# Kernel optimization log

Measured on AMD Instinct MI355X. Metric: run time of the kernel, lower is better.

The kernel has to match this reference:

```python
import jax, jax.numpy as jnp
import numpy as np

N, F, F_, H = 8192, 1024, 64, 4
LEAKY_ALPHA = 0.2
MASK_VAL = -1e10


def setup_inputs() -> dict:
    key = jax.random.key(0)
    k1, k2, k3, k4 = jax.random.split(key, 4)
    X = jax.random.normal(k1, (N, F), dtype=jnp.float32)
    # sparse-ish binary adjacency with self loops (A = A + I in the source script)
    A = (jax.random.uniform(k2, (N, N)) < 0.004).astype(jnp.float32)
    A = jnp.clip(A + jnp.eye(N, dtype=jnp.float32), 0.0, 1.0)
    W = jax.random.normal(k3, (H, F, F_), dtype=jnp.float32) * (1.0 / np.sqrt(F))
    attn_a = jax.random.normal(k4, (H, 2 * F_, 1), dtype=jnp.float32) * (1.0 / np.sqrt(2 * F_))
    bias = jnp.zeros((H, F_), dtype=jnp.float32)
    return {"X": X, "A": A, "W": W, "attn_a": attn_a, "bias": bias}


def reference(X, A, W, attn_a, bias):
    # features per head: [H, N, F_]
    feats = jnp.einsum('nf,hfk->hnk', X, W)
    # concat-score trick: [f_i, f_j] @ a == f_i @ a[:F_] + f_j @ a[F_:]
    a_self = attn_a[:, :F_, 0]   # [H, F_]
    a_neigh = attn_a[:, F_:, 0]  # [H, F_]
    s_self = jnp.einsum('hnk,hk->hn', feats, a_self)   # [H, N]
    s_neigh = jnp.einsum('hnk,hk->hn', feats, a_neigh)  # [H, N]
    scores = s_self[:, :, None] + s_neigh[:, None, :]   # [H, N, N]
    scores = jnp.where(scores > 0, scores, LEAKY_ALPHA * scores)  # LeakyReLU(0.2)
    scores = scores + MASK_VAL * (1.0 - A)[None]
    attn = jax.nn.softmax(scores, axis=-1)              # [H, N, N]
    # aggregate (dropout is identity at inference)
    out = jnp.einsum('hij,hjk->hik', attn, feats) + bias[:, None, :]  # [H, N, F_]
    out = jnp.transpose(out, (1, 0, 2)).reshape(X.shape[0], H * F_)   # concat heads
    return jax.nn.relu(out)
```

## Files before the change

kernel.cpp:

```cpp
#include <hip/hip_runtime.h>
#include <hip/hip_bf16.h>
#include <stdint.h>

#define NN 8192
#define FF 1024
#define FD 64
#define NH 4
#define CC 256
#define MAXE 192

typedef __attribute__((ext_vector_type(8))) short short8;
typedef __attribute__((ext_vector_type(4))) short short4v;
typedef __attribute__((ext_vector_type(4))) float f32x4;

__device__ __forceinline__ short bf16_rne(float f) {
    union { float f; uint32_t u; } v; v.f = f;
    uint32_t r = (v.u + 0x7FFFu + ((v.u >> 16) & 1u)) >> 16;
    return (short)(r & 0xFFFFu);
}
__device__ __forceinline__ float bf2f(short s) {
    union { uint32_t u; float f; } v; v.u = ((uint32_t)(uint16_t)s) << 16;
    return v.f;
}

__global__ __launch_bounds__(256) void scan_kernel(const float* __restrict__ A,
                                                   int* __restrict__ nbr,
                                                   int* __restrict__ cnt) {
    __shared__ int idx[MAXE];
    __shared__ int c;
    const int row = blockIdx.x;
    const int t = threadIdx.x;
    if (t == 0) c = 0;
    __syncthreads();
    const f32x4* A4 = (const f32x4*)(A + (size_t)row * NN);
    for (int r = 0; r < 8; ++r) {
        int c4 = r * 256 + t;
        f32x4 v = __builtin_nontemporal_load(&A4[c4]);
        if (v.x > 0.5f) { int p = atomicAdd(&c, 1); if (p < MAXE) idx[p] = c4 * 4 + 0; }
        if (v.y > 0.5f) { int p = atomicAdd(&c, 1); if (p < MAXE) idx[p] = c4 * 4 + 1; }
        if (v.z > 0.5f) { int p = atomicAdd(&c, 1); if (p < MAXE) idx[p] = c4 * 4 + 2; }
        if (v.w > 0.5f) { int p = atomicAdd(&c, 1); if (p < MAXE) idx[p] = c4 * 4 + 3; }
    }
    __syncthreads();
    int n = min(c, MAXE);
    if (t < n) nbr[row * MAXE + t] = idx[t];
    if (t == 0) cnt[row] = n;
}

__global__ __launch_bounds__(256) void wt_kernel(const float* __restrict__ W,
                                                 short* __restrict__ Wt) {
    int gid = blockIdx.x * 256 + threadIdx.x;
    int k = gid & 1023;
    int n = (gid >> 10) & 63;
    int h = gid >> 16;
    Wt[gid] = bf16_rne(W[(h << 16) + k * 64 + n]);
}

__global__ __launch_bounds__(256) void xb_kernel(const float* __restrict__ X,
                                                 short* __restrict__ Xb) {
    int gid = blockIdx.x * 256 + threadIdx.x;
    float4 v = ((const float4*)X)[gid];
    short4 o;
    o.x = bf16_rne(v.x); o.y = bf16_rne(v.y);
    o.z = bf16_rne(v.z); o.w = bf16_rne(v.w);
    ((short4*)Xb)[gid] = o;
}

__global__ __launch_bounds__(256) void gemm_kernel(const short* __restrict__ Xb,
                                                   const short* __restrict__ Wt,
                                                   const float* __restrict__ attn_a,
                                                   short* __restrict__ featb,
                                                   float* __restrict__ s_self,
                                                   float* __restrict__ s_neigh) {
    __shared__ short Xs[64 * 40];
    __shared__ short Ws[64 * 40];
    const int h  = blockIdx.x;
    const int m0 = blockIdx.y * 64;
    const int t  = threadIdx.x;
    const int wave = t >> 6, lane = t & 63;
    const int q = lane >> 4, nl = lane & 15;
    const int srow = t >> 2, sk8 = (t & 3) * 8;

    f32x4 acc0 = {0.f,0.f,0.f,0.f}, acc1 = {0.f,0.f,0.f,0.f};
    f32x4 acc2 = {0.f,0.f,0.f,0.f}, acc3 = {0.f,0.f,0.f,0.f};

    const short* Xp = Xb + (size_t)(m0 + srow) * FF + sk8;
    const short* Wp = Wt + (size_t)(h * 64 + srow) * FF + sk8;

    for (int k0 = 0; k0 < FF; k0 += 32) {
        short8 xv = *(const short8*)(Xp + k0);
        short8 wv = *(const short8*)(Wp + k0);
        *(short8*)(&Xs[srow * 40 + sk8]) = xv;
        *(short8*)(&Ws[srow * 40 + sk8]) = wv;
        __syncthreads();
        short8 a  = *(const short8*)(&Xs[(wave * 16 + nl) * 40 + q * 8]);
        short8 b0 = *(const short8*)(&Ws[( 0 + nl) * 40 + q * 8]);
        short8 b1 = *(const short8*)(&Ws[(16 + nl) * 40 + q * 8]);
        short8 b2 = *(const short8*)(&Ws[(32 + nl) * 40 + q * 8]);
        short8 b3 = *(const short8*)(&Ws[(48 + nl) * 40 + q * 8]);
        acc0 = __builtin_amdgcn_mfma_f32_16x16x32_bf16(a, b0, acc0, 0, 0, 0);
        acc1 = __builtin_amdgcn_mfma_f32_16x16x32_bf16(a, b1, acc1, 0, 0, 0);
        acc2 = __builtin_amdgcn_mfma_f32_16x16x32_bf16(a, b2, acc2, 0, 0, 0);
        acc3 = __builtin_amdgcn_mfma_f32_16x16x32_bf16(a, b3, acc3, 0, 0, 0);
        __syncthreads();
    }
    const int row = m0 + wave * 16 + q * 4;
    const int colbase = h * 64 + nl;
    for (int r = 0; r < 4; ++r) {
        short* fr = featb + (size_t)(row + r) * CC + colbase;
        fr[ 0] = bf16_rne(acc0[r]);
        fr[16] = bf16_rne(acc1[r]);
        fr[32] = bf16_rne(acc2[r]);
        fr[48] = bf16_rne(acc3[r]);
    }
    const float A0 = attn_a[h * 128 + nl],      A1 = attn_a[h * 128 + nl + 16];
    const float A2 = attn_a[h * 128 + nl + 32], A3 = attn_a[h * 128 + nl + 48];
    const float B0 = attn_a[h * 128 + 64 + nl],      B1 = attn_a[h * 128 + 64 + nl + 16];
    const float B2 = attn_a[h * 128 + 64 + nl + 32], B3 = attn_a[h * 128 + 64 + nl + 48];
    for (int r = 0; r < 4; ++r) {
        float ps = acc0[r] * A0 + acc1[r] * A1 + acc2[r] * A2 + acc3[r] * A3;
        float pn = acc0[r] * B0 + acc1[r] * B1 + acc2[r] * B2 + acc3[r] * B3;
        for (int off = 1; off < 16; off <<= 1) {
            ps += __shfl_xor(ps, off);
            pn += __shfl_xor(pn, off);
        }
        if (nl == 0) {
            s_self [h * NN + row + r] = ps;
            s_neigh[h * NN + row + r] = pn;
        }
    }
}

__global__ __launch_bounds__(256) void smax_kernel(const int* __restrict__ nbr,
                                                   const int* __restrict__ cnt,
                                                   const short* __restrict__ featb,
                                                   const float* __restrict__ s_self,
                                                   const float* __restrict__ s_neigh,
                                                   const float* __restrict__ bias,
                                                   float* __restrict__ out) {
    __shared__ int js[MAXE];
    __shared__ float ps[NH][MAXE];
    const int row = blockIdx.x;
    const int t = threadIdx.x;
    const int h = t >> 6, lane = t & 63;
    const int n = cnt[row];
    if (t < n) js[t] = nbr[row * MAXE + t];
    __syncthreads();

    const float si = s_self[h * NN + row];
    const float* snh = s_neigh + h * NN;

    float sc[3];
    #pragma unroll
    for (int i = 0; i < 3; ++i) {
        int e = lane + 64 * i;
        float s = -1e30f;
        if (e < n) {
            s = si + snh[js[e]];
            s = s > 0.f ? s : 0.2f * s;
        }
        sc[i] = s;
    }
    float m = fmaxf(sc[0], fmaxf(sc[1], sc[2]));
    for (int off = 1; off < 64; off <<= 1) m = fmaxf(m, __shfl_xor(m, off));

    float dsum = 0.f;
    #pragma unroll
    for (int i = 0; i < 3; ++i) {
        int e = lane + 64 * i;
        if (e < n) {
            float p = __expf(sc[i] - m);
            ps[h][e] = p;
            dsum += p;
        }
    }
    for (int off = 1; off < 64; off <<= 1) dsum += __shfl_xor(dsum, off);

    const int sub = lane >> 4;
    const int l16 = lane & 15;
    const short* fb = featb + h * 64 + l16 * 4;
    f32x4 acc = {0.f, 0.f, 0.f, 0.f};
    #pragma unroll 2
    for (int e = sub; e < n; e += 4) {
        int j = js[e];
        float p = ps[h][e];
        short4v f = *(const short4v*)(fb + (size_t)j * CC);
        acc[0] = fmaf(p, bf2f(f.x), acc[0]);
        acc[1] = fmaf(p, bf2f(f.y), acc[1]);
        acc[2] = fmaf(p, bf2f(f.z), acc[2]);
        acc[3] = fmaf(p, bf2f(f.w), acc[3]);
    }
    #pragma unroll
    for (int k = 0; k < 4; ++k) {
        acc[k] += __shfl_xor(acc[k], 16);
        acc[k] += __shfl_xor(acc[k], 32);
    }
    if (sub == 0) {
        float rd = 1.0f / dsum;
        f32x4 o;
        #pragma unroll
        for (int k = 0; k < 4; ++k)
            o[k] = fmaxf(acc[k] * rd + bias[h * 64 + l16 * 4 + k], 0.f);
        *(f32x4*)(out + (size_t)row * CC + h * 64 + l16 * 4) = o;
    }
}

extern "C" void kernel_launch(void* const* d_in, const int* in_sizes, int n_in,
                              void* d_out, int out_size, void* d_ws, size_t ws_size,
                              hipStream_t stream) {
    const float* X      = (const float*)d_in[0];
    const float* A      = (const float*)d_in[1];
    const float* W      = (const float*)d_in[2];
    const float* attn_a = (const float*)d_in[3];
    const float* bias   = (const float*)d_in[4];
    float* out = (float*)d_out;

    char* ws = (char*)d_ws;
    short* featb   = (short*)ws;
    float* s_self  = (float*)(ws + 4194304);
    float* s_neigh = (float*)(ws + 4325376);
    short* Wt      = (short*)(ws + 4456448);
    short* Xb      = (short*)(ws + 4980736);
    int*   nbr     = (int*)  (ws + 21757952);
    int*   cnt     = (int*)  (ws + 28049408);

    scan_kernel<<<NN, 256, 0, stream>>>(A, nbr, cnt);
    wt_kernel  <<<1024, 256, 0, stream>>>(W, Wt);
    xb_kernel  <<<8192, 256, 0, stream>>>(X, Xb);
    gemm_kernel<<<dim3(4, 128), 256, 0, stream>>>(Xb, Wt, attn_a, featb, s_self, s_neigh);
    smax_kernel<<<NN, 256, 0, stream>>>(nbr, cnt, featb, s_self, s_neigh, bias, out);
}
```

Before: 402.1 us.

## Fuse adjacency scan into softmax-aggregate kernel, dropping neighbor list buffer

The separate scan kernel that compacted each adjacency row into a neighbor index list is merged into the softmax/aggregation kernel, which now scans its row of A directly into shared memory. This removes one launch and the global write and reread of the neighbor list and counts. The score loops now iterate over a runtime chunk count instead of a fixed three. Dynamic indexing of the small score array may push it to scratch, and the A-read latency now sits on the same blocks as the gather work.

```diff
diff --git a/kernel.cpp b/kernel.cpp
--- a/kernel.cpp
+++ b/kernel.cpp
@@ -21,30 +21,6 @@
 __device__ __forceinline__ float bf2f(short s) {
     union { uint32_t u; float f; } v; v.u = ((uint32_t)(uint16_t)s) << 16;
     return v.f;
-}
-
-__global__ __launch_bounds__(256) void scan_kernel(const float* __restrict__ A,
-                                                   int* __restrict__ nbr,
-                                                   int* __restrict__ cnt) {
-    __shared__ int idx[MAXE];
-    __shared__ int c;
-    const int row = blockIdx.x;
-    const int t = threadIdx.x;
-    if (t == 0) c = 0;
-    __syncthreads();
-    const f32x4* A4 = (const f32x4*)(A + (size_t)row * NN);
-    for (int r = 0; r < 8; ++r) {
-        int c4 = r * 256 + t;
-        f32x4 v = __builtin_nontemporal_load(&A4[c4]);
-        if (v.x > 0.5f) { int p = atomicAdd(&c, 1); if (p < MAXE) idx[p] = c4 * 4 + 0; }
-        if (v.y > 0.5f) { int p = atomicAdd(&c, 1); if (p < MAXE) idx[p] = c4 * 4 + 1; }
-        if (v.z > 0.5f) { int p = atomicAdd(&c, 1); if (p < MAXE) idx[p] = c4 * 4 + 2; }
-        if (v.w > 0.5f) { int p = atomicAdd(&c, 1); if (p < MAXE) idx[p] = c4 * 4 + 3; }
-    }
-    __syncthreads();
-    int n = min(c, MAXE);
-    if (t < n) nbr[row * MAXE + t] = idx[t];
-    if (t == 0) cnt[row] = n;
 }
 
 __global__ __launch_bounds__(256) void wt_kernel(const float* __restrict__ W,
@@ -131,8 +107,7 @@
     }
 }
 
-__global__ __launch_bounds__(256) void smax_kernel(const int* __restrict__ nbr,
-                                                   const int* __restrict__ cnt,
+__global__ __launch_bounds__(256) void smax_kernel(const float* __restrict__ A,
                                                    const short* __restrict__ featb,
                                                    const float* __restrict__ s_self,
                                                    const float* __restrict__ s_neigh,
@@ -140,33 +115,45 @@
                                                    float* __restrict__ out) {
     __shared__ int js[MAXE];
     __shared__ float ps[NH][MAXE];
+    __shared__ int cs;
     const int row = blockIdx.x;
     const int t = threadIdx.x;
+    if (t == 0) cs = 0;
+    __syncthreads();
+
+    const f32x4* A4 = (const f32x4*)(A + (size_t)row * NN);
+    #pragma unroll
+    for (int r = 0; r < 8; ++r) {
+        int c4 = r * 256 + t;
+        f32x4 v = __builtin_nontemporal_load(&A4[c4]);
+        if (v.x > 0.5f) { int p = atomicAdd(&cs, 1); if (p < MAXE) js[p] = c4 * 4 + 0; }
+        if (v.y > 0.5f) { int p = atomicAdd(&cs, 1); if (p < MAXE) js[p] = c4 * 4 + 1; }
+        if (v.z > 0.5f) { int p = atomicAdd(&cs, 1); if (p < MAXE) js[p] = c4 * 4 + 2; }
+        if (v.w > 0.5f) { int p = atomicAdd(&cs, 1); if (p < MAXE) js[p] = c4 * 4 + 3; }
+    }
+    __syncthreads();
+    const int n = min(cs, MAXE);
     const int h = t >> 6, lane = t & 63;
-    const int n = cnt[row];
-    if (t < n) js[t] = nbr[row * MAXE + t];
-    __syncthreads();
 
     const float si = s_self[h * NN + row];
     const float* snh = s_neigh + h * NN;
 
     float sc[3];
     #pragma unroll
-    for (int i = 0; i < 3; ++i) {
+    for (int i = 0; i < 3; ++i) sc[i] = -1e30f;
+    const int nchunk = (n + 63) >> 6;
+    for (int i = 0; i < nchunk; ++i) {
         int e = lane + 64 * i;
-        float s = -1e30f;
         if (e < n) {
-            s = si + snh[js[e]];
-            s = s > 0.f ? s : 0.2f * s;
-        }
-        sc[i] = s;
+            float s = si + snh[js[e]];
+            sc[i] = s > 0.f ? s : 0.2f * s;
+        }
     }
     float m = fmaxf(sc[0], fmaxf(sc[1], sc[2]));
     for (int off = 1; off < 64; off <<= 1) m = fmaxf(m, __shfl_xor(m, off));
 
     float dsum = 0.f;
-    #pragma unroll
-    for (int i = 0; i < 3; ++i) {
+    for (int i = 0; i < nchunk; ++i) {
         int e = lane + 64 * i;
         if (e < n) {
             float p = __expf(sc[i] - m);
@@ -221,12 +208,9 @@
     float* s_neigh = (float*)(ws + 4325376);
     short* Wt      = (short*)(ws + 4456448);
     short* Xb      = (short*)(ws + 4980736);
-    int*   nbr     = (int*)  (ws + 21757952);
-    int*   cnt     = (int*)  (ws + 28049408);
-
-    scan_kernel<<<NN, 256, 0, stream>>>(A, nbr, cnt);
+
     wt_kernel  <<<1024, 256, 0, stream>>>(W, Wt);
     xb_kernel  <<<8192, 256, 0, stream>>>(X, Xb);
     gemm_kernel<<<dim3(4, 128), 256, 0, stream>>>(Xb, Wt, attn_a, featb, s_self, s_neigh);
-    smax_kernel<<<NN, 256, 0, stream>>>(nbr, cnt, featb, s_self, s_neigh, bias, out);
-}
+    smax_kernel<<<NN, 256, 0, stream>>>(A, featb, s_self, s_neigh, bias, out);
+}
```

Result: no change. 399.7 us (-0.6%).

## Fuse X bf16 conversion into GEMM and run adjacency scan in same launch

Applied to the files above, without the earlier changes.

Drops the separate X-to-bf16 kernel by converting fp32 X to bf16 inside the GEMM tile loads, and merges the adjacency scan into the GEMM launch as extra blocks so the two independent jobs run concurrently. The softmax score loop now covers only the neighbor chunks that exist. This removes a 32MB round trip for Xb and two launches, but the GEMM now reads twice as many bytes per tile and the scan and GEMM blocks compete for the same CUs.

```diff
diff --git a/kernel.cpp b/kernel.cpp
--- a/kernel.cpp
+++ b/kernel.cpp
@@ -8,6 +8,7 @@
 #define NH 4
 #define CC 256
 #define MAXE 192
+#define GEMM_BLOCKS 512
 
 typedef __attribute__((ext_vector_type(8))) short short8;
 typedef __attribute__((ext_vector_type(4))) short short4v;
@@ -21,30 +22,6 @@
 __device__ __forceinline__ float bf2f(short s) {
     union { uint32_t u; float f; } v; v.u = ((uint32_t)(uint16_t)s) << 16;
     return v.f;
-}
-
-__global__ __launch_bounds__(256) void scan_kernel(const float* __restrict__ A,
-                                                   int* __restrict__ nbr,
-                                                   int* __restrict__ cnt) {
-    __shared__ int idx[MAXE];
-    __shared__ int c;
-    const int row = blockIdx.x;
-    const int t = threadIdx.x;
-    if (t == 0) c = 0;
-    __syncthreads();
-    const f32x4* A4 = (const f32x4*)(A + (size_t)row * NN);
-    for (int r = 0; r < 8; ++r) {
-        int c4 = r * 256 + t;
-        f32x4 v = __builtin_nontemporal_load(&A4[c4]);
-        if (v.x > 0.5f) { int p = atomicAdd(&c, 1); if (p < MAXE) idx[p] = c4 * 4 + 0; }
-        if (v.y > 0.5f) { int p = atomicAdd(&c, 1); if (p < MAXE) idx[p] = c4 * 4 + 1; }
-        if (v.z > 0.5f) { int p = atomicAdd(&c, 1); if (p < MAXE) idx[p] = c4 * 4 + 2; }
-        if (v.w > 0.5f) { int p = atomicAdd(&c, 1); if (p < MAXE) idx[p] = c4 * 4 + 3; }
-    }
-    __syncthreads();
-    int n = min(c, MAXE);
-    if (t < n) nbr[row * MAXE + t] = idx[t];
-    if (t == 0) cnt[row] = n;
 }
 
 __global__ __launch_bounds__(256) void wt_kernel(const float* __restrict__ W,
@@ -56,27 +33,45 @@
     Wt[gid] = bf16_rne(W[(h << 16) + k * 64 + n]);
 }
 
-__global__ __launch_bounds__(256) void xb_kernel(const float* __restrict__ X,
-                                                 short* __restrict__ Xb) {
-    int gid = blockIdx.x * 256 + threadIdx.x;
-    float4 v = ((const float4*)X)[gid];
-    short4 o;
-    o.x = bf16_rne(v.x); o.y = bf16_rne(v.y);
-    o.z = bf16_rne(v.z); o.w = bf16_rne(v.w);
-    ((short4*)Xb)[gid] = o;
-}
-
-__global__ __launch_bounds__(256) void gemm_kernel(const short* __restrict__ Xb,
-                                                   const short* __restrict__ Wt,
-                                                   const float* __restrict__ attn_a,
-                                                   short* __restrict__ featb,
-                                                   float* __restrict__ s_self,
-                                                   float* __restrict__ s_neigh) {
+__global__ __launch_bounds__(256) void fused_kernel(const float* __restrict__ X,
+                                                    const short* __restrict__ Wt,
+                                                    const float* __restrict__ attn_a,
+                                                    const float* __restrict__ A,
+                                                    short* __restrict__ featb,
+                                                    float* __restrict__ s_self,
+                                                    float* __restrict__ s_neigh,
+                                                    int* __restrict__ nbr,
+                                                    int* __restrict__ cnt) {
     __shared__ short Xs[64 * 40];
     __shared__ short Ws[64 * 40];
-    const int h  = blockIdx.x;
-    const int m0 = blockIdx.y * 64;
-    const int t  = threadIdx.x;
+    __shared__ int idx[MAXE];
+    __shared__ int c;
+    const int bid = blockIdx.x;
+    const int t = threadIdx.x;
+
+    if (bid >= GEMM_BLOCKS) {
+        const int row = bid - GEMM_BLOCKS;
+        if (t == 0) c = 0;
+        __syncthreads();
+        const f32x4* A4 = (const f32x4*)(A + (size_t)row * NN);
+        #pragma unroll
+        for (int r = 0; r < 8; ++r) {
+            int c4 = r * 256 + t;
+            f32x4 v = __builtin_nontemporal_load(&A4[c4]);
+            if (v.x > 0.5f) { int p = atomicAdd(&c, 1); if (p < MAXE) idx[p] = c4 * 4 + 0; }
+            if (v.y > 0.5f) { int p = atomicAdd(&c, 1); if (p < MAXE) idx[p] = c4 * 4 + 1; }
+            if (v.z > 0.5f) { int p = atomicAdd(&c, 1); if (p < MAXE) idx[p] = c4 * 4 + 2; }
+            if (v.w > 0.5f) { int p = atomicAdd(&c, 1); if (p < MAXE) idx[p] = c4 * 4 + 3; }
+        }
+        __syncthreads();
+        int n = min(c, MAXE);
+        if (t < n) nbr[row * MAXE + t] = idx[t];
+        if (t == 0) cnt[row] = n;
+        return;
+    }
+
+    const int h  = bid & 3;
+    const int m0 = (bid >> 2) * 64;
     const int wave = t >> 6, lane = t & 63;
     const int q = lane >> 4, nl = lane & 15;
     const int srow = t >> 2, sk8 = (t & 3) * 8;
@@ -84,12 +79,18 @@
     f32x4 acc0 = {0.f,0.f,0.f,0.f}, acc1 = {0.f,0.f,0.f,0.f};
     f32x4 acc2 = {0.f,0.f,0.f,0.f}, acc3 = {0.f,0.f,0.f,0.f};
 
-    const short* Xp = Xb + (size_t)(m0 + srow) * FF + sk8;
+    const float* Xp = X + (size_t)(m0 + srow) * FF + sk8;
     const short* Wp = Wt + (size_t)(h * 64 + srow) * FF + sk8;
 
     for (int k0 = 0; k0 < FF; k0 += 32) {
-        short8 xv = *(const short8*)(Xp + k0);
+        float4 x0 = *(const float4*)(Xp + k0);
+        float4 x1 = *(const float4*)(Xp + k0 + 4);
         short8 wv = *(const short8*)(Wp + k0);
+        short8 xv;
+        xv[0] = bf16_rne(x0.x); xv[1] = bf16_rne(x0.y);
+        xv[2] = bf16_rne(x0.z); xv[3] = bf16_rne(x0.w);
+        xv[4] = bf16_rne(x1.x); xv[5] = bf16_rne(x1.y);
+        xv[6] = bf16_rne(x1.z); xv[7] = bf16_rne(x1.w);
         *(short8*)(&Xs[srow * 40 + sk8]) = xv;
         *(short8*)(&Ws[srow * 40 + sk8]) = wv;
         __syncthreads();
@@ -152,21 +153,20 @@
 
     float sc[3];
     #pragma unroll
-    for (int i = 0; i < 3; ++i) {
+    for (int i = 0; i < 3; ++i) sc[i] = -1e30f;
+    const int nchunk = (n + 63) >> 6;
+    for (int i = 0; i < nchunk; ++i) {
         int e = lane + 64 * i;
-        float s = -1e30f;
         if (e < n) {
-            s = si + snh[js[e]];
-            s = s > 0.f ? s : 0.2f * s;
-        }
-        sc[i] = s;
+            float s = si + snh[js[e]];
+            sc[i] = s > 0.f ? s : 0.2f * s;
+        }
     }
     float m = fmaxf(sc[0], fmaxf(sc[1], sc[2]));
     for (int off = 1; off < 64; off <<= 1) m = fmaxf(m, __shfl_xor(m, off));
 
     float dsum = 0.f;
-    #pragma unroll
-    for (int i = 0; i < 3; ++i) {
+    for (int i = 0; i < nchunk; ++i) {
         int e = lane + 64 * i;
         if (e < n) {
             float p = __expf(sc[i] - m);
@@ -220,13 +220,11 @@
     float* s_self  = (float*)(ws + 4194304);
     float* s_neigh = (float*)(ws + 4325376);
     short* Wt      = (short*)(ws + 4456448);
-    short* Xb      = (short*)(ws + 4980736);
-    int*   nbr     = (int*)  (ws + 21757952);
-    int*   cnt     = (int*)  (ws + 28049408);
-
-    scan_kernel<<<NN, 256, 0, stream>>>(A, nbr, cnt);
-    wt_kernel  <<<1024, 256, 0, stream>>>(W, Wt);
-    xb_kernel  <<<8192, 256, 0, stream>>>(X, Xb);
-    gemm_kernel<<<dim3(4, 128), 256, 0, stream>>>(Xb, Wt, attn_a, featb, s_self, s_neigh);
-    smax_kernel<<<NN, 256, 0, stream>>>(nbr, cnt, featb, s_self, s_neigh, bias, out);
-}
+    int*   nbr     = (int*)  (ws + 4980736);
+    int*   cnt     = (int*)  (ws + 11272192);
+
+    wt_kernel   <<<1024, 256, 0, stream>>>(W, Wt);
+    fused_kernel<<<GEMM_BLOCKS + NN, 256, 0, stream>>>(X, Wt, attn_a, A,
+                                                       featb, s_self, s_neigh, nbr, cnt);
+    smax_kernel <<<NN, 256, 0, stream>>>(nbr, cnt, featb, s_self, s_neigh, bias, out);
+}
```

Result: no change. 405.7 us (+0.9%).
